# Performance work log

Hardware: AMD Instinct MI355X
Metric: run time of the kernel (lower is better)

Reference implementation:

```python
import jax, jax.numpy as jnp
import numpy as np

TOP_K = 6
ROUTED_SCALE = 2.5

def setup_inputs() -> dict:
    key = jax.random.key(0)
    ks = jax.random.split(key, 8)
    T, H, I, E = 1024, 2048, 1024, 16
    Is = 2 * I  # shared expert intermediate = n_shared_experts * moe_intermediate_size
    s = 0.02
    return {
        "hidden_states": jax.random.normal(ks[0], (T, H), jnp.float32),
        "gate_w": jax.random.normal(ks[1], (E, H), jnp.float32) * s,          # ReplicatedLinear [out,in]
        "e_score_correction_bias": jax.random.normal(ks[2], (E,), jnp.float32) * s,
        "w1": jax.random.normal(ks[3], (E, 2 * I, H), jnp.float32) * s,       # merged gate_up per expert
        "w2": jax.random.normal(ks[4], (E, H, I), jnp.float32) * s,           # down proj per expert
        "shared_w1": jax.random.normal(ks[5], (2 * Is, H), jnp.float32) * s,  # shared gate_up
        "shared_w2": jax.random.normal(ks[6], (H, Is), jnp.float32) * s,      # shared down
    }

def _silu_and_mul(gu):
    g, u = jnp.split(gu, 2, axis=-1)
    return jax.nn.silu(g) * u

def _moe_forward(hidden_states, gate_w, e_score_correction_bias, w1, w2, shared_w1, shared_w2):
    T, H = hidden_states.shape
    E = gate_w.shape[0]
    # shared expert path (Dots1MLP)
    shared_out = _silu_and_mul(hidden_states @ shared_w1.T) @ shared_w2.T  # [T,H]
    # gating in fp32 (moe_gating_fp32=True)
    router_logits = hidden_states.astype(jnp.float32) @ gate_w.astype(jnp.float32).T  # [T,E]
    # noaux_tc routing: sigmoid scores + correction bias for selection, raw sigmoid for weights
    scores = jax.nn.sigmoid(router_logits)
    choice = scores + e_score_correction_bias[None, :]
    _, topk_idx = jax.lax.top_k(choice, TOP_K)                              # [T,k]
    topk_w = jnp.take_along_axis(scores, topk_idx, axis=1)                  # [T,k]
    topk_w = topk_w / jnp.sum(topk_w, axis=-1, keepdims=True)
    topk_w = topk_w * ROUTED_SCALE
    # dense combine weights [T,E] (top-k slots per token, rest zero)
    route_w = jnp.zeros((T, E), jnp.float32)
    route_w = route_w.at[jnp.arange(T)[:, None], topk_idx].set(topk_w)
    # expert MLPs (computed for all experts, masked by routing weights)
    gu = jnp.einsum('th,egh->teg', hidden_states, w1)                       # [T,E,2I]
    h = _silu_and_mul(gu)                                                   # [T,E,I]
    routed_out = jnp.einsum('tei,ehi,te->th', h, w2, route_w.astype(hidden_states.dtype))
    return routed_out + shared_out                                          # [T,H]

def reference(hidden_states, gate_w, e_score_correction_bias, w1, w2, shared_w1, shared_w2):
    return _moe_forward(hidden_states, gate_w, e_score_correction_bias, w1, w2, shared_w1, shared_w2)
```

## Files before the change

kernel.cpp:

```cpp
#include <hip/hip_runtime.h>
#include <hip/hip_bf16.h>

#define T_TOK 1024
#define NEXP 16
#define HD 2048
#define TOPK 6

typedef __attribute__((ext_vector_type(8))) short short8;
typedef __attribute__((ext_vector_type(4))) float floatx4;

__device__ __forceinline__ short f2bf(float f) {
    unsigned u = __builtin_bit_cast(unsigned, f);
    u += 0x7FFFu + ((u >> 16) & 1u);
    return (short)(u >> 16);
}

typedef __attribute__((address_space(1))) void gvoid;
typedef __attribute__((address_space(3))) void lvoid;
__device__ __forceinline__ void gload_lds16(const void* g, void* l) {
    __builtin_amdgcn_global_load_lds((gvoid*)g, (lvoid*)l, 16, 0, 0);
}

#define WAITCNT_VM4 0x0F74
#define WAITCNT_VM0 0x0F70

__global__ __launch_bounds__(256) void router_cvt(
    const float* __restrict__ X, const float* __restrict__ GW,
    const float* __restrict__ bias, int* __restrict__ counts,
    int* __restrict__ lists, int* __restrict__ tok_e,
    int* __restrict__ tok_pos, float* __restrict__ tok_w,
    const float* __restrict__ W1, const float* __restrict__ SW1,
    short* __restrict__ Xb, short* __restrict__ W1b, short* __restrict__ SW1b)
{
    if (blockIdx.x < 256) {
        const int wave = threadIdx.x >> 6;
        const int l = threadIdx.x & 63;
        const int t = blockIdx.x * 4 + wave;
        const float* x = X + (size_t)t * HD;
        float acc[NEXP];
#pragma unroll
        for (int e = 0; e < NEXP; ++e) acc[e] = 0.f;
        for (int k = l; k < HD; k += 64) {
            const float xv = x[k];
#pragma unroll
            for (int e = 0; e < NEXP; ++e) acc[e] += xv * GW[e * HD + k];
        }
#pragma unroll
        for (int e = 0; e < NEXP; ++e) {
            float v = acc[e];
#pragma unroll
            for (int m = 32; m >= 1; m >>= 1) v += __shfl_xor(v, m, 64);
            acc[e] = v;
        }
        if (l == 0) {
            float s[NEXP], choice[NEXP];
#pragma unroll
            for (int e = 0; e < NEXP; ++e) {
                s[e] = 1.f / (1.f + __expf(-acc[e]));
                choice[e] = s[e] + bias[e];
            }
            int idx[TOPK]; float wv[TOPK]; float wsum = 0.f;
            bool used[NEXP];
#pragma unroll
            for (int e = 0; e < NEXP; ++e) used[e] = false;
            for (int j = 0; j < TOPK; ++j) {
                float best = -1e30f; int bi = 0;
                for (int e = 0; e < NEXP; ++e)
                    if (!used[e] && choice[e] > best) { best = choice[e]; bi = e; }
                used[bi] = true; idx[j] = bi; wv[j] = s[bi]; wsum += s[bi];
            }
            const float scale = 2.5f / wsum;
            for (int j = 0; j < TOPK; ++j) {
                const int e = idx[j];
                const int pos = atomicAdd(&counts[e], 1);
                lists[e * T_TOK + pos] = t;
                tok_e[t * TOPK + j] = e;
                tok_pos[t * TOPK + j] = pos;
                tok_w[t * TOPK + j] = wv[j] * scale;
            }
        }
        return;
    }
    const int C0 = 262144;
    const int C1 = C0 + 8388608;
    const int C2 = C1 + 1048576;
    const int stride = (gridDim.x - 256) * 256;
#pragma unroll 2
    for (int i = (int)(blockIdx.x - 256) * 256 + (int)threadIdx.x; i < C2;
         i += stride) {
        const float* s; short* d; int l;
        if (i < C0)      { s = X;   d = Xb;   l = i; }
        else if (i < C1) { s = W1;  d = W1b;  l = i - C0; }
        else             { s = SW1; d = SW1b; l = i - C1; }
        const floatx4 v0 = ((const floatx4*)s)[2 * l];
        const floatx4 v1 = ((const floatx4*)s)[2 * l + 1];
        short8 o;
        o[0] = f2bf(v0[0]); o[1] = f2bf(v0[1]); o[2] = f2bf(v0[2]); o[3] = f2bf(v0[3]);
        o[4] = f2bf(v1[0]); o[5] = f2bf(v1[1]); o[6] = f2bf(v1[2]); o[7] = f2bf(v1[3]);
        ((short8*)d)[l] = o;
    }
}

__global__ __launch_bounds__(256) void offsets_descs(
    const int* __restrict__ counts, int* __restrict__ offs,
    int* __restrict__ gu, int* __restrict__ gu_n,
    int* __restrict__ dn, int* __restrict__ dn_n)
{
    __shared__ int base_gu[NEXP], base_dn[NEXP], nys[NEXP];
    if (threadIdx.x == 0) {
        int a = 0, bg = 256, bd = 128;
        for (int e = 0; e < NEXP; ++e) {
            offs[e] = a; a += counts[e];
            const int ny = (counts[e] + 127) >> 7;
            nys[e] = ny; base_gu[e] = bg; base_dn[e] = bd;
            bg += ny * 16; bd += ny * 16;
        }
        *gu_n = bg; *dn_n = bd;
    }
    __syncthreads();
    for (int i = threadIdx.x; i < 256; i += 256)
        gu[i] = (NEXP << 16) | ((i >> 5) << 8) | (i & 31);
    for (int i = threadIdx.x; i < 128; i += 256)
        dn[i] = (NEXP << 16) | ((i >> 4) << 8) | (i & 15);
    for (int e = 0; e < NEXP; ++e) {
        const int nt = nys[e] * 16;
        for (int i = threadIdx.x; i < nt; i += 256) {
            const int v = (e << 16) | ((i >> 4) << 8) | (i & 15);
            gu[base_gu[e] + i] = v;
            dn[base_dn[e] + i] = v;
        }
    }
}

__global__ __launch_bounds__(256) void gateup3(
    const short* __restrict__ Xbf, const short* __restrict__ W1bf,
    const short* __restrict__ SW1bf,
    const int* __restrict__ counts, const int* __restrict__ offs,
    const int* __restrict__ lists, const int* __restrict__ descs,
    const int* __restrict__ ndesc,
    short* __restrict__ h_r, short* __restrict__ h_s,
    const float* __restrict__ W2f, const float* __restrict__ SW2f,
    short* __restrict__ W2b, short* __restrict__ SW2b)
{
    __shared__ short sA[3][128][32];
    __shared__ short sB[3][128][32];
    if (blockIdx.x >= 1280) {
        const int CW0 = 4194304;
        const int CW1 = CW0 + 524288;
        const int stride = ((int)gridDim.x - 1280) * 256;
#pragma unroll 2
        for (int i = ((int)blockIdx.x - 1280) * 256 + (int)threadIdx.x;
             i < CW1; i += stride) {
            const float* s; short* d; int l;
            if (i < CW0) { s = W2f;  d = W2b;  l = i; }
            else         { s = SW2f; d = SW2b; l = i - CW0; }
            const floatx4 v0 = __builtin_nontemporal_load(((const floatx4*)s) + 2 * l);
            const floatx4 v1 = __builtin_nontemporal_load(((const floatx4*)s) + 2 * l + 1);
            short8 o;
            o[0] = f2bf(v0[0]); o[1] = f2bf(v0[1]); o[2] = f2bf(v0[2]); o[3] = f2bf(v0[3]);
            o[4] = f2bf(v1[0]); o[5] = f2bf(v1[1]); o[6] = f2bf(v1[2]); o[7] = f2bf(v1[3]);
            ((short8*)d)[l] = o;
        }
        return;
    }
    if ((int)blockIdx.x >= *ndesc) return;
    const int d = descs[blockIdx.x];
    const int z = d >> 16, yb = (d >> 8) & 255, xb = d & 255;
    const bool shx = (z == NEXP);
    const int cnt = shx ? T_TOK : counts[z];
    const int m0 = yb * 128;
    if (m0 >= cnt) return;
    const int Ih = shx ? 2048 : 1024;
    const int i0 = xb * 64;
    const short* W = shx ? SW1bf : (W1bf + (size_t)z * 2048 * HD);
    short* Hout = shx ? h_s : h_r;
    const int hbase = shx ? 0 : offs[z];

    const int tid = threadIdx.x;
    const int wave = tid >> 6, lane = tid & 63;
    const int srow0 = wave * 32 + (lane >> 2);
    const int srow1 = srow0 + 16;
    const int scol = ((lane & 3) ^ ((lane >> 3) & 3)) * 8;

    int ar0 = m0 + srow0; if (ar0 > cnt - 1) ar0 = cnt - 1;
    int ar1 = m0 + srow1; if (ar1 > cnt - 1) ar1 = cnt - 1;
    const int tok0 = shx ? ar0 : lists[z * T_TOK + ar0];
    const int tok1 = shx ? ar1 : lists[z * T_TOK + ar1];
    const short* ag0 = Xbf + (size_t)tok0 * HD + scol;
    const short* ag1 = Xbf + (size_t)tok1 * HD + scol;
    const int br0 = (srow0 < 64) ? (i0 + srow0) : (Ih + i0 + srow0 - 64);
    const int br1 = (srow1 < 64) ? (i0 + srow1) : (Ih + i0 + srow1 - 64);
    const short* bg0 = W + (size_t)br0 * HD + scol;
    const short* bg1 = W + (size_t)br1 * HD + scol;

    const int wx = wave & 1, wy = wave >> 1;
    const int l15 = lane & 15, l4 = lane >> 4;
    const int fcol = (l4 ^ ((l15 >> 1) & 3)) * 8;

    floatx4 acc[4][4];
#pragma unroll
    for (int a = 0; a < 4; ++a)
#pragma unroll
        for (int b = 0; b < 4; ++b) acc[a][b] = (floatx4){0.f, 0.f, 0.f, 0.f};

    const int nsteps = HD / 32;
#pragma unroll
    for (int pb = 0; pb < 2; ++pb) {
        const int off = pb * 32;
        gload_lds16(ag0 + off, &sA[pb][wave * 32][0]);
        gload_lds16(ag1 + off, &sA[pb][wave * 32 + 16][0]);
        gload_lds16(bg0 + off, &sB[pb][wave * 32][0]);
        gload_lds16(bg1 + off, &sB[pb][wave * 32 + 16][0]);
    }

    int p = 0, q = 2;
    for (int s = 0; s < nsteps; ++s) {
        if (s + 1 < nsteps) __builtin_amdgcn_s_waitcnt(WAITCNT_VM4);
        else                __builtin_amdgcn_s_waitcnt(WAITCNT_VM0);
        __builtin_amdgcn_s_barrier();
        if (s + 2 < nsteps) {
            const int off = (s + 2) * 32;
            gload_lds16(ag0 + off, &sA[q][wave * 32][0]);
            gload_lds16(ag1 + off, &sA[q][wave * 32 + 16][0]);
            gload_lds16(bg0 + off, &sB[q][wave * 32][0]);
            gload_lds16(bg1 + off, &sB[q][wave * 32 + 16][0]);
        }
        short8 af[4], bfr[4];
#pragma unroll
        for (int mc = 0; mc < 4; ++mc)
            af[mc] = *(const short8*)&sA[p][wy * 64 + mc * 16 + l15][fcol];
#pragma unroll
        for (int cb = 0; cb < 4; ++cb) {
            const int br = ((cb < 2) ? 0 : 64) + wx * 32 + (cb & 1) * 16 + l15;
            bfr[cb] = *(const short8*)&sB[p][br][fcol];
        }
#pragma unroll
        for (int mc = 0; mc < 4; ++mc)
#pragma unroll
            for (int cb = 0; cb < 4; ++cb)
                acc[mc][cb] = __builtin_amdgcn_mfma_f32_16x16x32_bf16(
                    af[mc], bfr[cb], acc[mc][cb], 0, 0, 0);
        p = (p == 2) ? 0 : p + 1;
        q = (q == 2) ? 0 : q + 1;
    }

#pragma unroll
    for (int mc = 0; mc < 4; ++mc)
#pragma unroll
        for (int cb = 0; cb < 2; ++cb)
#pragma unroll
            for (int r = 0; r < 4; ++r) {
                const int mrel = wy * 64 + mc * 16 + l4 * 4 + r;
                if (m0 + mrel < cnt) {
                    const float g = acc[mc][cb][r];
                    const float u = acc[mc][cb + 2][r];
                    const float h = g / (1.f + __expf(-g)) * u;
                    const int col = i0 + wx * 32 + cb * 16 + l15;
                    Hout[(size_t)(hbase + m0 + mrel) * Ih + col] = f2bf(h);
                }
            }
}

__global__ __launch_bounds__(256) void down3(
    const short* __restrict__ h_r, const short* __restrict__ h_s,
    const short* __restrict__ W2bf, const short* __restrict__ SW2bf,
    const int* __restrict__ counts, const int* __restrict__ offs,
    const int* __restrict__ descs, const int* __restrict__ ndesc,
    float* __restrict__ h2, float* __restrict__ sh_out)
{
    __shared__ short sA[3][128][32];
    __shared__ short sB[3][128][32];
    if ((int)blockIdx.x >= *ndesc) return;
    const int d = descs[blockIdx.x];
    const int z = d >> 16, yb = (d >> 8) & 255, xb = d & 255;
    const bool shx = (z == NEXP);
    const int cnt = shx ? T_TOK : counts[z];
    const int m0 = yb * 128;
    if (m0 >= cnt) return;
    const int Kih = shx ? 2048 : 1024;
    const int n0 = xb * 128;
    const short* A = shx ? h_s : h_r;
    const short* W = shx ? SW2bf : (W2bf + (size_t)z * HD * 1024);
    float* outb = shx ? sh_out : h2;
    const int hbase = shx ? 0 : offs[z];

    const int tid = threadIdx.x;
    const int wave = tid >> 6, lane = tid & 63;
    const int srow0 = wave * 32 + (lane >> 2);
    const int srow1 = srow0 + 16;
    const int scol = ((lane & 3) ^ ((lane >> 3) & 3)) * 8;

    int ar0 = m0 + srow0; if (ar0 > cnt - 1) ar0 = cnt - 1;
    int ar1 = m0 + srow1; if (ar1 > cnt - 1) ar1 = cnt - 1;
    const short* ag0 = A + (size_t)(hbase + ar0) * Kih + scol;
    const short* ag1 = A + (size_t)(hbase + ar1) * Kih + scol;
    const short* bg0 = W + (size_t)(n0 + srow0) * Kih + scol;
    const short* bg1 = W + (size_t)(n0 + srow1) * Kih + scol;

    const int wx = wave & 1, wy = wave >> 1;
    const int l15 = lane & 15, l4 = lane >> 4;
    const int fcol = (l4 ^ ((l15 >> 1) & 3)) * 8;

    floatx4 acc[4][4];
#pragma unroll
    for (int a = 0; a < 4; ++a)
#pragma unroll
        for (int b = 0; b < 4; ++b) acc[a][b] = (floatx4){0.f, 0.f, 0.f, 0.f};

    const int nsteps = Kih / 32;
#pragma unroll
    for (int pb = 0; pb < 2; ++pb) {
        const int off = pb * 32;
        gload_lds16(ag0 + off, &sA[pb][wave * 32][0]);
        gload_lds16(ag1 + off, &sA[pb][wave * 32 + 16][0]);
        gload_lds16(bg0 + off, &sB[pb][wave * 32][0]);
        gload_lds16(bg1 + off, &sB[pb][wave * 32 + 16][0]);
    }

    int p = 0, q = 2;
    for (int s = 0; s < nsteps; ++s) {
        if (s + 1 < nsteps) __builtin_amdgcn_s_waitcnt(WAITCNT_VM4);
        else                __builtin_amdgcn_s_waitcnt(WAITCNT_VM0);
        __builtin_amdgcn_s_barrier();
        if (s + 2 < nsteps) {
            const int off = (s + 2) * 32;
            gload_lds16(ag0 + off, &sA[q][wave * 32][0]);
            gload_lds16(ag1 + off, &sA[q][wave * 32 + 16][0]);
            gload_lds16(bg0 + off, &sB[q][wave * 32][0]);
            gload_lds16(bg1 + off, &sB[q][wave * 32 + 16][0]);
        }
        short8 af[4], bfr[4];
#pragma unroll
        for (int mc = 0; mc < 4; ++mc)
            af[mc] = *(const short8*)&sA[p][wy * 64 + mc * 16 + l15][fcol];
#pragma unroll
        for (int cb = 0; cb < 4; ++cb)
            bfr[cb] = *(const short8*)&sB[p][wx * 64 + cb * 16 + l15][fcol];
#pragma unroll
        for (int mc = 0; mc < 4; ++mc)
#pragma unroll
            for (int cb = 0; cb < 4; ++cb)
                acc[mc][cb] = __builtin_amdgcn_mfma_f32_16x16x32_bf16(
                    af[mc], bfr[cb], acc[mc][cb], 0, 0, 0);
        p = (p == 2) ? 0 : p + 1;
        q = (q == 2) ? 0 : q + 1;
    }

#pragma unroll
    for (int mc = 0; mc < 4; ++mc)
#pragma unroll
        for (int r = 0; r < 4; ++r) {
            const int mrel = wy * 64 + mc * 16 + l4 * 4 + r;
            if (m0 + mrel >= cnt) continue;
            float* orow = outb + (size_t)(hbase + m0 + mrel) * HD + n0 + wx * 64 + l15;
#pragma unroll
            for (int cb = 0; cb < 4; ++cb)
                orow[cb * 16] = acc[mc][cb][r];
        }
}

__global__ __launch_bounds__(256) void combine_kernel(
    const float* __restrict__ h2, const float* __restrict__ sh_out,
    const int* __restrict__ offs, const int* __restrict__ tok_e,
    const int* __restrict__ tok_pos, const float* __restrict__ tok_w,
    float* __restrict__ out)
{
    const int t = blockIdx.x;
    int rows[TOPK]; float w[TOPK];
#pragma unroll
    for (int j = 0; j < TOPK; ++j) {
        const int e = tok_e[t * TOPK + j];
        rows[j] = offs[e] + tok_pos[t * TOPK + j];
        w[j] = tok_w[t * TOPK + j];
    }
    for (int c = threadIdx.x * 4; c < HD; c += 256 * 4) {
        float4 acc = *(const float4*)(sh_out + (size_t)t * HD + c);
#pragma unroll
        for (int j = 0; j < TOPK; ++j) {
            const float4 v = *(const float4*)(h2 + (size_t)rows[j] * HD + c);
            acc.x += w[j] * v.x; acc.y += w[j] * v.y;
            acc.z += w[j] * v.z; acc.w += w[j] * v.w;
        }
        *(float4*)(out + (size_t)t * HD + c) = acc;
    }
}

extern "C" void kernel_launch(void* const* d_in, const int* in_sizes, int n_in,
                              void* d_out, int out_size, void* d_ws, size_t ws_size,
                              hipStream_t stream) {
    const float* X    = (const float*)d_in[0];
    const float* GW   = (const float*)d_in[1];
    const float* BIAS = (const float*)d_in[2];
    const float* W1   = (const float*)d_in[3];
    const float* W2   = (const float*)d_in[4];
    const float* SW1  = (const float*)d_in[5];
    const float* SW2  = (const float*)d_in[6];
    float* out = (float*)d_out;

    char* ws = (char*)d_ws;
    int*   counts  = (int*)(ws + 0);
    int*   offs    = (int*)(ws + 64);
    int*   lists   = (int*)(ws + 256);
    int*   tok_e   = (int*)(ws + 65792);
    int*   tok_pos = (int*)(ws + 90368);
    float* tok_w   = (float*)(ws + 114944);
    int*   gu_n    = (int*)(ws + 139776);
    int*   dn_n    = (int*)(ws + 139780);
    int*   gu_desc = (int*)(ws + 139840);
    int*   dn_desc = (int*)(ws + 145024);
    short* h_r     = (short*)(ws + 262144);
    short* h_s     = (short*)(ws + 12845056);
    float* h2      = (float*)(ws + 17039360);
    float* sh_out  = (float*)(ws + 67371008);
    short* Xbf     = (short*)(ws + 75759616);
    short* W1bf    = (short*)(ws + 79953920);
    short* W2bf    = (short*)(ws + 214171648);
    short* SW1bf   = (short*)(ws + 281280512);
    short* SW2bf   = (short*)(ws + 298057728);
    const size_t WS_NEEDED = 306446336;
    if (ws_size < WS_NEEDED) return;

    hipMemsetAsync(counts, 0, 64, stream);
    router_cvt<<<4352, 256, 0, stream>>>(X, GW, BIAS, counts, lists,
                                         tok_e, tok_pos, tok_w,
                                         W1, SW1, Xbf, W1bf, SW1bf);
    offsets_descs<<<1, 256, 0, stream>>>(counts, offs, gu_desc, gu_n,
                                         dn_desc, dn_n);

    gateup3<<<3328, 256, 0, stream>>>(Xbf, W1bf, SW1bf, counts, offs, lists,
                                      gu_desc, gu_n, h_r, h_s,
                                      W2, SW2, W2bf, SW2bf);
    down3<<<1152, 256, 0, stream>>>(h_r, h_s, W2bf, SW2bf, counts, offs,
                                    dn_desc, dn_n, h2, sh_out);
    combine_kernel<<<T_TOK, 256, 0, stream>>>(
        h2, sh_out, offs, tok_e, tok_pos, tok_w, out);
}
```

Measured before the change: 747.8 us.

## Fuse fp32-to-bf16 weight conversion of W1/SW1 into gate-up GEMM B-loads

The separate pre-pass that converted W1 and shared W1 to bf16 is removed. The gate-up GEMM now loads those fp32 weights through registers, packs them with v_cvt_pk_bf16_f32 and writes them to swizzled LDS, in a restructured two-step pipeline with explicit waitcnts. This avoids writing the bf16 weight copy and reading it back. In exchange each tile reads twice as many weight bytes and spends extra VALU work and register pressure on conversion. Weights that several row tiles share also get converted more than once.

```diff
diff --git a/kernel.cpp b/kernel.cpp
--- a/kernel.cpp
+++ b/kernel.cpp
@@ -8,6 +8,7 @@
 
 typedef __attribute__((ext_vector_type(8))) short short8;
 typedef __attribute__((ext_vector_type(4))) float floatx4;
+typedef __attribute__((ext_vector_type(4))) unsigned uintx4;
 
 __device__ __forceinline__ short f2bf(float f) {
     unsigned u = __builtin_bit_cast(unsigned, f);
@@ -15,89 +16,87 @@
     return (short)(u >> 16);
 }
 
+__device__ __forceinline__ unsigned cvt_pk_bf16(float a, float b) {
+    unsigned r;
+    asm("v_cvt_pk_bf16_f32 %0, %1, %2" : "=v"(r) : "v"(a), "v"(b));
+    return r;
+}
+
 typedef __attribute__((address_space(1))) void gvoid;
 typedef __attribute__((address_space(3))) void lvoid;
 __device__ __forceinline__ void gload_lds16(const void* g, void* l) {
     __builtin_amdgcn_global_load_lds((gvoid*)g, (lvoid*)l, 16, 0, 0);
 }
 
-#define WAITCNT_VM4 0x0F74
-#define WAITCNT_VM0 0x0F70
-
-__global__ __launch_bounds__(256) void router_cvt(
+#define WC_VM6        0x0F76
+#define WC_VM4        0x0F74
+#define WC_VM2        0x0F72
+#define WC_VM0        0x0F70
+#define WC_LGKM0      0xC07F
+#define WC_LGKM0_VM4  0x0074
+
+__global__ __launch_bounds__(256) void router_xc(
     const float* __restrict__ X, const float* __restrict__ GW,
     const float* __restrict__ bias, int* __restrict__ counts,
     int* __restrict__ lists, int* __restrict__ tok_e,
     int* __restrict__ tok_pos, float* __restrict__ tok_w,
-    const float* __restrict__ W1, const float* __restrict__ SW1,
-    short* __restrict__ Xb, short* __restrict__ W1b, short* __restrict__ SW1b)
+    short* __restrict__ Xb)
 {
-    if (blockIdx.x < 256) {
-        const int wave = threadIdx.x >> 6;
-        const int l = threadIdx.x & 63;
-        const int t = blockIdx.x * 4 + wave;
-        const float* x = X + (size_t)t * HD;
-        float acc[NEXP];
-#pragma unroll
-        for (int e = 0; e < NEXP; ++e) acc[e] = 0.f;
-        for (int k = l; k < HD; k += 64) {
-            const float xv = x[k];
-#pragma unroll
-            for (int e = 0; e < NEXP; ++e) acc[e] += xv * GW[e * HD + k];
-        }
-#pragma unroll
-        for (int e = 0; e < NEXP; ++e) {
-            float v = acc[e];
-#pragma unroll
-            for (int m = 32; m >= 1; m >>= 1) v += __shfl_xor(v, m, 64);
-            acc[e] = v;
-        }
-        if (l == 0) {
-            float s[NEXP], choice[NEXP];
-#pragma unroll
-            for (int e = 0; e < NEXP; ++e) {
-                s[e] = 1.f / (1.f + __expf(-acc[e]));
-                choice[e] = s[e] + bias[e];
-            }
-            int idx[TOPK]; float wv[TOPK]; float wsum = 0.f;
-            bool used[NEXP];
-#pragma unroll
-            for (int e = 0; e < NEXP; ++e) used[e] = false;
-            for (int j = 0; j < TOPK; ++j) {
-                float best = -1e30f; int bi = 0;
-                for (int e = 0; e < NEXP; ++e)
-                    if (!used[e] && choice[e] > best) { best = choice[e]; bi = e; }
-                used[bi] = true; idx[j] = bi; wv[j] = s[bi]; wsum += s[bi];
-            }
-            const float scale = 2.5f / wsum;
-            for (int j = 0; j < TOPK; ++j) {
-                const int e = idx[j];
-                const int pos = atomicAdd(&counts[e], 1);
-                lists[e * T_TOK + pos] = t;
-                tok_e[t * TOPK + j] = e;
-                tok_pos[t * TOPK + j] = pos;
-                tok_w[t * TOPK + j] = wv[j] * scale;
-            }
-        }
-        return;
-    }
-    const int C0 = 262144;
-    const int C1 = C0 + 8388608;
-    const int C2 = C1 + 1048576;
-    const int stride = (gridDim.x - 256) * 256;
-#pragma unroll 2
-    for (int i = (int)(blockIdx.x - 256) * 256 + (int)threadIdx.x; i < C2;
-         i += stride) {
-        const float* s; short* d; int l;
-        if (i < C0)      { s = X;   d = Xb;   l = i; }
-        else if (i < C1) { s = W1;  d = W1b;  l = i - C0; }
-        else             { s = SW1; d = SW1b; l = i - C1; }
-        const floatx4 v0 = ((const floatx4*)s)[2 * l];
-        const floatx4 v1 = ((const floatx4*)s)[2 * l + 1];
+    if (blockIdx.x >= 256) {
+        const int i = ((int)blockIdx.x - 256) * 256 + (int)threadIdx.x;
+        const floatx4 v0 = ((const floatx4*)X)[2 * i];
+        const floatx4 v1 = ((const floatx4*)X)[2 * i + 1];
         short8 o;
         o[0] = f2bf(v0[0]); o[1] = f2bf(v0[1]); o[2] = f2bf(v0[2]); o[3] = f2bf(v0[3]);
         o[4] = f2bf(v1[0]); o[5] = f2bf(v1[1]); o[6] = f2bf(v1[2]); o[7] = f2bf(v1[3]);
-        ((short8*)d)[l] = o;
+        ((short8*)Xb)[i] = o;
+        return;
+    }
+    const int wave = threadIdx.x >> 6;
+    const int l = threadIdx.x & 63;
+    const int t = blockIdx.x * 4 + wave;
+    const float* x = X + (size_t)t * HD;
+    float acc[NEXP];
+#pragma unroll
+    for (int e = 0; e < NEXP; ++e) acc[e] = 0.f;
+    for (int k = l; k < HD; k += 64) {
+        const float xv = x[k];
+#pragma unroll
+        for (int e = 0; e < NEXP; ++e) acc[e] += xv * GW[e * HD + k];
+    }
+#pragma unroll
+    for (int e = 0; e < NEXP; ++e) {
+        float v = acc[e];
+#pragma unroll
+        for (int m = 32; m >= 1; m >>= 1) v += __shfl_xor(v, m, 64);
+        acc[e] = v;
+    }
+    if (l == 0) {
+        float s[NEXP], choice[NEXP];
+#pragma unroll
+        for (int e = 0; e < NEXP; ++e) {
+            s[e] = 1.f / (1.f + __expf(-acc[e]));
+            choice[e] = s[e] + bias[e];
+        }
+        int idx[TOPK]; float wv[TOPK]; float wsum = 0.f;
+        bool used[NEXP];
+#pragma unroll
+        for (int e = 0; e < NEXP; ++e) used[e] = false;
+        for (int j = 0; j < TOPK; ++j) {
+            float best = -1e30f; int bi = 0;
+            for (int e = 0; e < NEXP; ++e)
+                if (!used[e] && choice[e] > best) { best = choice[e]; bi = e; }
+            used[bi] = true; idx[j] = bi; wv[j] = s[bi]; wsum += s[bi];
+        }
+        const float scale = 2.5f / wsum;
+        for (int j = 0; j < TOPK; ++j) {
+            const int e = idx[j];
+            const int pos = atomicAdd(&counts[e], 1);
+            lists[e * T_TOK + pos] = t;
+            tok_e[t * TOPK + j] = e;
+            tok_pos[t * TOPK + j] = pos;
+            tok_w[t * TOPK + j] = wv[j] * scale;
+        }
     }
 }
 
@@ -132,9 +131,9 @@
     }
 }
 
-__global__ __launch_bounds__(256) void gateup3(
-    const short* __restrict__ Xbf, const short* __restrict__ W1bf,
-    const short* __restrict__ SW1bf,
+__global__ __launch_bounds__(256) void gateup_f32(
+    const short* __restrict__ Xbf,
+    const float* __restrict__ W1f, const float* __restrict__ SW1f,
     const int* __restrict__ counts, const int* __restrict__ offs,
     const int* __restrict__ lists, const int* __restrict__ descs,
     const int* __restrict__ ndesc,
@@ -172,7 +171,7 @@
     if (m0 >= cnt) return;
     const int Ih = shx ? 2048 : 1024;
     const int i0 = xb * 64;
-    const short* W = shx ? SW1bf : (W1bf + (size_t)z * 2048 * HD);
+    const float* W = shx ? SW1f : (W1f + (size_t)z * 2048 * HD);
     short* Hout = shx ? h_s : h_r;
     const int hbase = shx ? 0 : offs[z];
 
@@ -181,17 +180,19 @@
     const int srow0 = wave * 32 + (lane >> 2);
     const int srow1 = srow0 + 16;
     const int scol = ((lane & 3) ^ ((lane >> 3) & 3)) * 8;
-
     int ar0 = m0 + srow0; if (ar0 > cnt - 1) ar0 = cnt - 1;
     int ar1 = m0 + srow1; if (ar1 > cnt - 1) ar1 = cnt - 1;
     const int tok0 = shx ? ar0 : lists[z * T_TOK + ar0];
     const int tok1 = shx ? ar1 : lists[z * T_TOK + ar1];
     const short* ag0 = Xbf + (size_t)tok0 * HD + scol;
     const short* ag1 = Xbf + (size_t)tok1 * HD + scol;
-    const int br0 = (srow0 < 64) ? (i0 + srow0) : (Ih + i0 + srow0 - 64);
-    const int br1 = (srow1 < 64) ? (i0 + srow1) : (Ih + i0 + srow1 - 64);
-    const short* bg0 = W + (size_t)br0 * HD + scol;
-    const short* bg1 = W + (size_t)br1 * HD + scol;
+
+    const int r0 = tid >> 2, c0 = tid & 3;
+    const int r1 = r0 + 64;
+    const int sw = (r0 >> 1) & 3;
+    const int bcol = (c0 ^ sw) * 8;
+    const float* bsrc0 = W + (size_t)(i0 + r0) * HD + c0 * 8;
+    const float* bsrc1 = W + (size_t)(Ih + i0 + r0) * HD + c0 * 8;
 
     const int wx = wave & 1, wy = wave >> 1;
     const int l15 = lane & 15, l4 = lane >> 4;
@@ -203,45 +204,72 @@
 #pragma unroll
         for (int b = 0; b < 4; ++b) acc[a][b] = (floatx4){0.f, 0.f, 0.f, 0.f};
 
+#define BLOAD(d0, d1, d2, d3, s_) do {                                   \
+        const float* p0_ = bsrc0 + (size_t)(s_) * 32;                    \
+        const float* p1_ = bsrc1 + (size_t)(s_) * 32;                    \
+        d0 = *(const floatx4*)(p0_);  d1 = *(const floatx4*)(p0_ + 4);   \
+        d2 = *(const floatx4*)(p1_);  d3 = *(const floatx4*)(p1_ + 4);   \
+    } while (0)
+
+#define BWRITE(buf_, v0, v1, v2, v3) do {                                \
+        uintx4 w0, w1;                                                   \
+        w0[0] = cvt_pk_bf16(v0[0], v0[1]); w0[1] = cvt_pk_bf16(v0[2], v0[3]); \
+        w0[2] = cvt_pk_bf16(v1[0], v1[1]); w0[3] = cvt_pk_bf16(v1[2], v1[3]); \
+        w1[0] = cvt_pk_bf16(v2[0], v2[1]); w1[1] = cvt_pk_bf16(v2[2], v2[3]); \
+        w1[2] = cvt_pk_bf16(v3[0], v3[1]); w1[3] = cvt_pk_bf16(v3[2], v3[3]); \
+        *(uintx4*)&sB[buf_][r0][bcol] = w0;                              \
+        *(uintx4*)&sB[buf_][r1][bcol] = w1;                              \
+    } while (0)
+
+#define AGLOAD(buf_, s_) do {                                            \
+        gload_lds16(ag0 + (s_) * 32, &sA[buf_][wave * 32][0]);           \
+        gload_lds16(ag1 + (s_) * 32, &sA[buf_][wave * 32 + 16][0]);      \
+    } while (0)
+
+#define GUSTEP(pp) do {                                                  \
+        short8 af[4], bfr[4];                                            \
+        _Pragma("unroll") for (int mc = 0; mc < 4; ++mc)                 \
+            af[mc] = *(const short8*)&sA[pp][wy * 64 + mc * 16 + l15][fcol]; \
+        _Pragma("unroll") for (int cb = 0; cb < 4; ++cb) {               \
+            const int br = ((cb < 2) ? 0 : 64) + wx * 32 + (cb & 1) * 16 + l15; \
+            bfr[cb] = *(const short8*)&sB[pp][br][fcol]; }               \
+        _Pragma("unroll") for (int mc = 0; mc < 4; ++mc)                 \
+        _Pragma("unroll") for (int cb = 0; cb < 4; ++cb)                 \
+            acc[mc][cb] = __builtin_amdgcn_mfma_f32_16x16x32_bf16(       \
+                af[mc], bfr[cb], acc[mc][cb], 0, 0, 0);                  \
+    } while (0)
+
     const int nsteps = HD / 32;
-#pragma unroll
-    for (int pb = 0; pb < 2; ++pb) {
-        const int off = pb * 32;
-        gload_lds16(ag0 + off, &sA[pb][wave * 32][0]);
-        gload_lds16(ag1 + off, &sA[pb][wave * 32 + 16][0]);
-        gload_lds16(bg0 + off, &sB[pb][wave * 32][0]);
-        gload_lds16(bg1 + off, &sB[pb][wave * 32 + 16][0]);
-    }
-
-    int p = 0, q = 2;
-    for (int s = 0; s < nsteps; ++s) {
-        if (s + 1 < nsteps) __builtin_amdgcn_s_waitcnt(WAITCNT_VM4);
-        else                __builtin_amdgcn_s_waitcnt(WAITCNT_VM0);
+    floatx4 a0, a1, a2, a3, b0, b1, b2, b3;
+    BLOAD(a0, a1, a2, a3, 0);
+    AGLOAD(0, 0);
+    BLOAD(b0, b1, b2, b3, 1);
+    __builtin_amdgcn_s_waitcnt(WC_VM6);
+    BWRITE(0, a0, a1, a2, a3);
+    __builtin_amdgcn_s_waitcnt(WC_LGKM0_VM4);
+    __builtin_amdgcn_s_barrier();
+    AGLOAD(1, 1);
+
+    int p = 0;
+    for (int s = 0; s < nsteps; s += 2) {
+        if (s + 2 < nsteps) BLOAD(a0, a1, a2, a3, s + 2);
+        if (s + 2 < nsteps) __builtin_amdgcn_s_waitcnt(WC_VM6);
+        else                __builtin_amdgcn_s_waitcnt(WC_VM2);
+        BWRITE((p + 1) % 3, b0, b1, b2, b3);
+        __builtin_amdgcn_s_waitcnt(WC_LGKM0);
         __builtin_amdgcn_s_barrier();
-        if (s + 2 < nsteps) {
-            const int off = (s + 2) * 32;
-            gload_lds16(ag0 + off, &sA[q][wave * 32][0]);
-            gload_lds16(ag1 + off, &sA[q][wave * 32 + 16][0]);
-            gload_lds16(bg0 + off, &sB[q][wave * 32][0]);
-            gload_lds16(bg1 + off, &sB[q][wave * 32 + 16][0]);
-        }
-        short8 af[4], bfr[4];
-#pragma unroll
-        for (int mc = 0; mc < 4; ++mc)
-            af[mc] = *(const short8*)&sA[p][wy * 64 + mc * 16 + l15][fcol];
-#pragma unroll
-        for (int cb = 0; cb < 4; ++cb) {
-            const int br = ((cb < 2) ? 0 : 64) + wx * 32 + (cb & 1) * 16 + l15;
-            bfr[cb] = *(const short8*)&sB[p][br][fcol];
-        }
-#pragma unroll
-        for (int mc = 0; mc < 4; ++mc)
-#pragma unroll
-            for (int cb = 0; cb < 4; ++cb)
-                acc[mc][cb] = __builtin_amdgcn_mfma_f32_16x16x32_bf16(
-                    af[mc], bfr[cb], acc[mc][cb], 0, 0, 0);
-        p = (p == 2) ? 0 : p + 1;
-        q = (q == 2) ? 0 : q + 1;
+        if (s + 2 < nsteps) AGLOAD((p + 2) % 3, s + 2);
+        GUSTEP(p);
+        p = (p + 1) % 3;
+        if (s + 3 < nsteps) BLOAD(b0, b1, b2, b3, s + 3);
+        if (s + 3 < nsteps) __builtin_amdgcn_s_waitcnt(WC_VM6);
+        else                __builtin_amdgcn_s_waitcnt(WC_VM0);
+        if (s + 2 < nsteps) BWRITE((p + 1) % 3, a0, a1, a2, a3);
+        __builtin_amdgcn_s_waitcnt(WC_LGKM0);
+        __builtin_amdgcn_s_barrier();
+        if (s + 3 < nsteps) AGLOAD((p + 2) % 3, s + 3);
+        GUSTEP(p);
+        p = (p + 1) % 3;
     }
 
 #pragma unroll
@@ -259,6 +287,10 @@
                     Hout[(size_t)(hbase + m0 + mrel) * Ih + col] = f2bf(h);
                 }
             }
+#undef BLOAD
+#undef BWRITE
+#undef AGLOAD
+#undef GUSTEP
 }
 
 __global__ __launch_bounds__(256) void down3(
@@ -319,8 +351,8 @@
 
     int p = 0, q = 2;
     for (int s = 0; s < nsteps; ++s) {
-        if (s + 1 < nsteps) __builtin_amdgcn_s_waitcnt(WAITCNT_VM4);
-        else                __builtin_amdgcn_s_waitcnt(WAITCNT_VM0);
+        if (s + 1 < nsteps) __builtin_amdgcn_s_waitcnt(WC_VM4);
+        else                __builtin_amdgcn_s_waitcnt(WC_VM0);
         __builtin_amdgcn_s_barrier();
         if (s + 2 < nsteps) {
             const int off = (s + 2) * 32;
@@ -413,23 +445,20 @@
     float* h2      = (float*)(ws + 17039360);
     float* sh_out  = (float*)(ws + 67371008);
     short* Xbf     = (short*)(ws + 75759616);
-    short* W1bf    = (short*)(ws + 79953920);
     short* W2bf    = (short*)(ws + 214171648);
-    short* SW1bf   = (short*)(ws + 281280512);
     short* SW2bf   = (short*)(ws + 298057728);
     const size_t WS_NEEDED = 306446336;
     if (ws_size < WS_NEEDED) return;
 
     hipMemsetAsync(counts, 0, 64, stream);
-    router_cvt<<<4352, 256, 0, stream>>>(X, GW, BIAS, counts, lists,
-                                         tok_e, tok_pos, tok_w,
-                                         W1, SW1, Xbf, W1bf, SW1bf);
+    router_xc<<<1280, 256, 0, stream>>>(X, GW, BIAS, counts, lists,
+                                        tok_e, tok_pos, tok_w, Xbf);
     offsets_descs<<<1, 256, 0, stream>>>(counts, offs, gu_desc, gu_n,
                                          dn_desc, dn_n);
 
-    gateup3<<<3328, 256, 0, stream>>>(Xbf, W1bf, SW1bf, counts, offs, lists,
-                                      gu_desc, gu_n, h_r, h_s,
-                                      W2, SW2, W2bf, SW2bf);
+    gateup_f32<<<3328, 256, 0, stream>>>(Xbf, W1, SW1, counts, offs, lists,
+                                         gu_desc, gu_n, h_r, h_s,
+                                         W2, SW2, W2bf, SW2bf);
     down3<<<1152, 256, 0, stream>>>(h_r, h_s, W2bf, SW2bf, counts, offs,
                                     dn_desc, dn_n, h2, sh_out);
     combine_kernel<<<T_TOK, 256, 0, stream>>>(
```

Measured after the change: 771.1 us. +3.1%, slower.
